# Performance work log

Measured on AMD Instinct MI355X. Metric: run time of the kernel, lower is better.

Reference implementation:

```python
import jax, jax.numpy as jnp
import numpy as np

COMMITMENT_COST = 0.25
NUM_EMBEDDINGS = 512
EMBEDDING_DIM = 64


def setup_inputs() -> dict:
    key = jax.random.key(0)
    k1, k2 = jax.random.split(key)
    B, T = 64, 1024
    inputs = jax.random.normal(k1, (B, T, EMBEDDING_DIM), dtype=jnp.float32)
    # matches nn.Embedding init uniform_(-1/K, 1/K)
    embedding = jax.random.uniform(
        k2, (NUM_EMBEDDINGS, EMBEDDING_DIM), dtype=jnp.float32,
        minval=-1.0 / NUM_EMBEDDINGS, maxval=1.0 / NUM_EMBEDDINGS)
    return {"inputs": inputs, "embedding": embedding}


def reference(inputs, embedding):
    B = inputs.shape[0]
    K, D = embedding.shape
    flat = inputs.reshape(-1, D)  # [N, D]
    # squared-euclidean distances [N, K] (same expansion as torch source)
    distances = (
        jnp.sum(flat * flat, axis=1, keepdims=True)
        + jnp.sum(embedding * embedding, axis=1)
        - 2.0 * flat @ embedding.T
    )
    idx = jnp.argmin(distances, axis=1)  # [N]
    # one-hot @ embedding  ==  gather
    quantized = embedding[idx].reshape(inputs.shape)

    e_latent_loss = jnp.mean((jax.lax.stop_gradient(quantized) - inputs) ** 2)
    q_latent_loss = jnp.mean((quantized - jax.lax.stop_gradient(inputs)) ** 2)
    loss = q_latent_loss + COMMITMENT_COST * e_latent_loss

    # straight-through estimator
    quantized_st = inputs + jax.lax.stop_gradient(quantized - inputs)

    # avg_probs = mean of one-hot encodings == histogram of indices / N
    counts = jax.ops.segment_sum(
        jnp.ones(flat.shape[0], dtype=jnp.float32), idx, num_segments=K)
    avg_probs = counts / flat.shape[0]
    perplexity = jnp.exp(-jnp.sum(avg_probs * jnp.log(avg_probs + 1e-10)))

    indices_for_transformer = idx.reshape(B, -1)
    return loss, quantized_st, perplexity, indices_for_transformer
```

## Files before the change

kernel.cpp:

```cpp
#include <hip/hip_runtime.h>
#include <math.h>

#define D 64
#define K 512
#define BLOCK 256
#define ROWS 128
#define KT 128
#define NKT (K / KT)
#define NPART 32


__device__ __forceinline__ float np_sumsq64(const float* v) {
#pragma clang fp contract(off)
    float r[8];
#pragma unroll
    for (int m = 0; m < 8; ++m) r[m] = v[m] * v[m];
#pragma unroll
    for (int i = 8; i < 64; i += 8) {
#pragma unroll
        for (int m = 0; m < 8; ++m) r[m] = r[m] + v[i + m] * v[i + m];
    }
    return ((r[0] + r[1]) + (r[2] + r[3])) + ((r[4] + r[5]) + (r[6] + r[7]));
}

__global__ __launch_bounds__(BLOCK, 2) void vq_fused(
    const float* __restrict__ x, const float* __restrict__ emb,
    float* __restrict__ q_out, float* __restrict__ idx_out,
    float* __restrict__ block_sums, int* __restrict__ part_hist, int N)
{
    __shared__ float4 xs4[ROWS * 16];
    __shared__ float4 es4[KT * 16];
    __shared__ float sx_s[ROWS];
    __shared__ float se_s[KT];
    __shared__ int hist[K];
    __shared__ float red[BLOCK / 64];

    const int tid = threadIdx.x;
    const int rg = tid & 15;
    const int cg = tid >> 4;
    const int rowbase = blockIdx.x * ROWS;

    for (int k2 = tid; k2 < K; k2 += BLOCK) hist[k2] = 0;

    const float4* xsrc = (const float4*)(x + (size_t)rowbase * D);
#pragma unroll
    for (int i = 0; i < (ROWS * 16) / BLOCK; ++i) {
        int f = tid + i * BLOCK;
        int row = f >> 4, jc = f & 15;
        xs4[row * 16 + (jc ^ ((row >> 3) & 7))] = xsrc[f];
    }
    __syncthreads();

    if (tid < ROWS) {
        float xr[D];
        const int sw = (tid >> 3) & 7;
#pragma unroll
        for (int jc = 0; jc < 16; ++jc) {
            float4 v = xs4[tid * 16 + (jc ^ sw)];
            xr[4 * jc + 0] = v.x; xr[4 * jc + 1] = v.y;
            xr[4 * jc + 2] = v.z; xr[4 * jc + 3] = v.w;
        }
        sx_s[tid] = np_sumsq64(xr);
    }

    float bd[8], bkf[8];
#pragma unroll
    for (int r = 0; r < 8; ++r) { bd[r] = INFINITY; bkf[r] = 0.f; }

    const int xbase = rg * 8, ebase = cg * 8;
    const int swx0 = rg & 7, swe0 = cg & 7;

    for (int kt = 0; kt < NKT; ++kt) {
        const float4* esrc = (const float4*)(emb + (size_t)kt * KT * D);
#pragma unroll
        for (int i = 0; i < (KT * 16) / BLOCK; ++i) {
            int f = tid + i * BLOCK;
            int row = f >> 4, jc = f & 15;
            es4[row * 16 + (jc ^ ((row >> 3) & 7))] = esrc[f];
        }
        __syncthreads();

        if (tid < KT) {
            float er[D];
            const int sw = (tid >> 3) & 7;
#pragma unroll
            for (int jc = 0; jc < 16; ++jc) {
                float4 v = es4[tid * 16 + (jc ^ sw)];
                er[4 * jc + 0] = v.x; er[4 * jc + 1] = v.y;
                er[4 * jc + 2] = v.z; er[4 * jc + 3] = v.w;
            }
            se_s[tid] = np_sumsq64(er);
        }

        float acc[8][8];
#pragma unroll
        for (int r = 0; r < 8; ++r)
#pragma unroll
            for (int c = 0; c < 8; ++c) acc[r][c] = 0.f;

#pragma unroll 2
        for (int jc = 0; jc < 16; ++jc) {
            float4 xa[8], eb[8];
#pragma unroll
            for (int r = 0; r < 8; ++r)
                xa[r] = xs4[(xbase + r) * 16 + (jc ^ swx0)];
#pragma unroll
            for (int c = 0; c < 8; ++c)
                eb[c] = es4[(ebase + c) * 16 + (jc ^ swe0)];
#pragma unroll
            for (int r = 0; r < 8; ++r)
#pragma unroll
                for (int c = 0; c < 8; ++c) {
                    acc[r][c] = fmaf(xa[r].x, eb[c].x, acc[r][c]);
                    acc[r][c] = fmaf(xa[r].y, eb[c].y, acc[r][c]);
                    acc[r][c] = fmaf(xa[r].z, eb[c].z, acc[r][c]);
                    acc[r][c] = fmaf(xa[r].w, eb[c].w, acc[r][c]);
                }
        }
        __syncthreads();

        const int kglob = kt * KT + ebase;
        float sev[8];
#pragma unroll
        for (int c = 0; c < 8; ++c) sev[c] = se_s[ebase + c];
#pragma unroll
        for (int r = 0; r < 8; ++r) {
            float sxv = sx_s[xbase + r];
#pragma unroll
            for (int c = 0; c < 8; ++c) {
                float dcur = (sxv + sev[c]) - 2.0f * acc[r][c];
                if (dcur < bd[r]) { bd[r] = dcur; bkf[r] = (float)(kglob + c); }
            }
        }
    }

    __syncthreads();
    float2* bests = (float2*)es4;
#pragma unroll
    for (int r = 0; r < 8; ++r)
        bests[(xbase + r) * 16 + cg] = make_float2(bd[r], bkf[r]);
    __syncthreads();

    float s = 0.f;
    if (tid < ROWS) {
        float bdd = INFINITY, bjf = 1e30f;
#pragma unroll
        for (int g = 0; g < 16; ++g) {
            float2 p = bests[tid * 16 + g];
            if (p.x < bdd || (p.x == bdd && p.y < bjf)) { bdd = p.x; bjf = p.y; }
        }
        const int bi = (int)bjf;
        atomicAdd(&hist[bi], 1);

        const int rowg = rowbase + tid;
        const float4* ep = (const float4*)(emb + (size_t)bi * D);
        float4* qp = (float4*)(q_out + (size_t)rowg * D);
        const int sw = (tid >> 3) & 7;
#pragma unroll
        for (int jc = 0; jc < 16; ++jc) {
            float4 xv = xs4[tid * 16 + (jc ^ sw)];
            float4 e  = ep[jc];
            float dx0 = e.x - xv.x, dx1 = e.y - xv.y;
            float dx2 = e.z - xv.z, dx3 = e.w - xv.w;
            s = fmaf(dx0, dx0, s);
            s = fmaf(dx1, dx1, s);
            s = fmaf(dx2, dx2, s);
            s = fmaf(dx3, dx3, s);
            float4 qs;
            qs.x = xv.x + dx0; qs.y = xv.y + dx1;
            qs.z = xv.z + dx2; qs.w = xv.w + dx3;
            qp[jc] = qs;
        }
        idx_out[rowg] = (float)bi;
    }

    for (int off = 32; off; off >>= 1) s += __shfl_down(s, off, 64);
    if ((tid & 63) == 0) red[tid >> 6] = s;
    __syncthreads();
    if (tid == 0) {
        float t = 0.f;
#pragma unroll
        for (int w = 0; w < BLOCK / 64; ++w) t += red[w];
        block_sums[blockIdx.x] = t;
    }
    const int part = (int)(blockIdx.x & (NPART - 1));
    for (int k2 = tid; k2 < K; k2 += BLOCK) {
        int h = hist[k2];
        if (h) atomicAdd(&part_hist[part * K + k2], h);
    }
}

__global__ __launch_bounds__(512) void vq_finalize(
    const float* __restrict__ block_sums, int nblocks,
    const int* __restrict__ part_hist, float* __restrict__ out_loss,
    float* __restrict__ out_perp, float inv_nelem, float inv_rows)
{
    const int tid = threadIdx.x;
    double ls = 0.0;
    for (int i = tid; i < nblocks; i += 512) ls += (double)block_sums[i];
    int c = 0;
#pragma unroll
    for (int pp = 0; pp < NPART; ++pp) c += part_hist[pp * K + tid];
    double ps = 0.0;
    {
        float p = (float)c * inv_rows;
        ps = (double)(p * logf(p + 1e-10f));
    }
    for (int off = 32; off; off >>= 1) {
        ls += __shfl_down(ls, off, 64);
        ps += __shfl_down(ps, off, 64);
    }
    __shared__ double l8[8], p8[8];
    if ((tid & 63) == 0) { l8[tid >> 6] = ls; p8[tid >> 6] = ps; }
    __syncthreads();
    if (tid == 0) {
        double L = 0.0, P = 0.0;
#pragma unroll
        for (int w = 0; w < 8; ++w) { L += l8[w]; P += p8[w]; }
        *out_loss = 1.25f * (float)(L * (double)inv_nelem);
        *out_perp = expf((float)(-P));
    }
}

extern "C" void kernel_launch(void* const* d_in, const int* in_sizes, int n_in,
                              void* d_out, int out_size, void* d_ws, size_t ws_size,
                              hipStream_t stream) {
    const float* x   = (const float*)d_in[0];
    const float* emb = (const float*)d_in[1];
    const int N = in_sizes[0] / D;
    const int nblocks = N / ROWS;

    float* out      = (float*)d_out;
    float* loss_out = out;
    float* q_out    = out + 1;
    float* perp_out = out + 1 + (size_t)N * D;
    float* idx_out  = perp_out + 1;

    float* block_sums = (float*)d_ws;
    int*   part_hist  = (int*)((char*)d_ws + (((size_t)nblocks * 4 + 255) & ~(size_t)255));

    hipMemsetAsync(part_hist, 0, NPART * K * sizeof(int), stream);
    vq_fused<<<nblocks, BLOCK, 0, stream>>>(x, emb, q_out, idx_out,
                                            block_sums, part_hist, N);
    vq_finalize<<<1, 512, 0, stream>>>(block_sums, nblocks, part_hist,
                                       loss_out, perp_out,
                                       1.0f / (float)((size_t)N * D),
                                       1.0f / (float)N);
}
```

Baseline: 139.8 us.

## Fuse finalize into main kernel, stream codebook from global, shuffle-reduce argmin

Removes the shared-memory codebook tile staging and per-tile barriers. Each thread now reads its 8 codebook rows straight from global/L2 and precomputes all codebook norms up front. The per-row argmin is reduced across column groups with wave shuffles instead of a 16-way shared-memory scan. The separate finalize kernel is folded into the main kernel through a last-block-done atomic counter, which saves one launch. The cost is that direct global loads of the codebook may have higher latency than LDS reads, and each block redundantly computes all 512 codebook norms.

Result: slower. 204.9 us (+46.6%).

```diff
diff --git a/kernel.cpp b/kernel.cpp
--- a/kernel.cpp
+++ b/kernel.cpp
@@ -5,8 +5,7 @@
 #define K 512
 #define BLOCK 256
 #define ROWS 128
-#define KT 128
-#define NKT (K / KT)
+#define NTILE 4
 #define NPART 32
 
 
@@ -26,16 +25,23 @@
 __global__ __launch_bounds__(BLOCK, 2) void vq_fused(
     const float* __restrict__ x, const float* __restrict__ emb,
     float* __restrict__ q_out, float* __restrict__ idx_out,
-    float* __restrict__ block_sums, int* __restrict__ part_hist, int N)
+    float* __restrict__ block_sums, int* __restrict__ part_hist,
+    int* __restrict__ done_ctr,
+    float* __restrict__ out_loss, float* __restrict__ out_perp,
+    float inv_nelem, float inv_rows)
 {
     __shared__ float4 xs4[ROWS * 16];
-    __shared__ float4 es4[KT * 16];
     __shared__ float sx_s[ROWS];
-    __shared__ float se_s[KT];
+    __shared__ float se_s[K];
+    __shared__ float2 bests[4 * ROWS];
     __shared__ int hist[K];
-    __shared__ float red[BLOCK / 64];
+    __shared__ float redf[BLOCK / 64];
+    __shared__ double l8[BLOCK / 64], p8[BLOCK / 64];
+    __shared__ int flag_s;
 
     const int tid = threadIdx.x;
+    const int lane = tid & 63;
+    const int wv = tid >> 6;
     const int rg = tid & 15;
     const int cg = tid >> 4;
     const int rowbase = blockIdx.x * ROWS;
@@ -49,104 +55,134 @@
         int row = f >> 4, jc = f & 15;
         xs4[row * 16 + (jc ^ ((row >> 3) & 7))] = xsrc[f];
     }
-    __syncthreads();
+
+#pragma unroll
+    for (int t = 0; t < K / BLOCK; ++t) {
+        const int k0 = tid + t * BLOCK;
+        float er[D];
+        const float4* e4 = (const float4*)(emb + (size_t)k0 * D);
+#pragma unroll
+        for (int j = 0; j < 16; ++j) {
+            float4 v = e4[j];
+            er[4 * j + 0] = v.x; er[4 * j + 1] = v.y;
+            er[4 * j + 2] = v.z; er[4 * j + 3] = v.w;
+        }
+        se_s[k0] = np_sumsq64(er);
+    }
 
     if (tid < ROWS) {
         float xr[D];
-        const int sw = (tid >> 3) & 7;
-#pragma unroll
+        const float4* xp = (const float4*)(x + (size_t)(rowbase + tid) * D);
+#pragma unroll
+        for (int j = 0; j < 16; ++j) {
+            float4 v = xp[j];
+            xr[4 * j + 0] = v.x; xr[4 * j + 1] = v.y;
+            xr[4 * j + 2] = v.z; xr[4 * j + 3] = v.w;
+        }
+        sx_s[tid] = np_sumsq64(xr);
+    }
+    __syncthreads();
+
+    float bd[8], bkf[8];
+#pragma unroll
+    for (int r = 0; r < 8; ++r) { bd[r] = INFINITY; bkf[r] = 0.f; }
+
+    const int xbase = rg * 8;
+    const int sw = rg & 7;
+
+#pragma unroll 1
+    for (int t = 0; t < NTILE; ++t) {
+        const int kb = t * 128 + cg * 8;
+        const float4* ebase = (const float4*)(emb + (size_t)kb * D);
+
+        float acc[8][8];
+#pragma unroll
+        for (int r = 0; r < 8; ++r)
+#pragma unroll
+            for (int c = 0; c < 8; ++c) acc[r][c] = 0.f;
+
+#pragma unroll 4
         for (int jc = 0; jc < 16; ++jc) {
-            float4 v = xs4[tid * 16 + (jc ^ sw)];
-            xr[4 * jc + 0] = v.x; xr[4 * jc + 1] = v.y;
-            xr[4 * jc + 2] = v.z; xr[4 * jc + 3] = v.w;
-        }
-        sx_s[tid] = np_sumsq64(xr);
-    }
-
-    float bd[8], bkf[8];
-#pragma unroll
-    for (int r = 0; r < 8; ++r) { bd[r] = INFINITY; bkf[r] = 0.f; }
-
-    const int xbase = rg * 8, ebase = cg * 8;
-    const int swx0 = rg & 7, swe0 = cg & 7;
-
-    for (int kt = 0; kt < NKT; ++kt) {
-        const float4* esrc = (const float4*)(emb + (size_t)kt * KT * D);
-#pragma unroll
-        for (int i = 0; i < (KT * 16) / BLOCK; ++i) {
-            int f = tid + i * BLOCK;
-            int row = f >> 4, jc = f & 15;
-            es4[row * 16 + (jc ^ ((row >> 3) & 7))] = esrc[f];
-        }
-        __syncthreads();
-
-        if (tid < KT) {
-            float er[D];
-            const int sw = (tid >> 3) & 7;
-#pragma unroll
-            for (int jc = 0; jc < 16; ++jc) {
-                float4 v = es4[tid * 16 + (jc ^ sw)];
-                er[4 * jc + 0] = v.x; er[4 * jc + 1] = v.y;
-                er[4 * jc + 2] = v.z; er[4 * jc + 3] = v.w;
+            float4 xa[8];
+#pragma unroll
+            for (int r = 0; r < 8; ++r)
+                xa[r] = xs4[(xbase + r) * 16 + (jc ^ sw)];
+#pragma unroll
+            for (int c = 0; c < 8; ++c) {
+                const float4 ev = ebase[c * 16 + jc];
+                acc[0][c] = fmaf(xa[0].x, ev.x, acc[0][c]);
+                acc[1][c] = fmaf(xa[1].x, ev.x, acc[1][c]);
+                acc[2][c] = fmaf(xa[2].x, ev.x, acc[2][c]);
+                acc[3][c] = fmaf(xa[3].x, ev.x, acc[3][c]);
+                acc[4][c] = fmaf(xa[4].x, ev.x, acc[4][c]);
+                acc[5][c] = fmaf(xa[5].x, ev.x, acc[5][c]);
+                acc[6][c] = fmaf(xa[6].x, ev.x, acc[6][c]);
+                acc[7][c] = fmaf(xa[7].x, ev.x, acc[7][c]);
+                acc[0][c] = fmaf(xa[0].y, ev.y, acc[0][c]);
+                acc[1][c] = fmaf(xa[1].y, ev.y, acc[1][c]);
+                acc[2][c] = fmaf(xa[2].y, ev.y, acc[2][c]);
+                acc[3][c] = fmaf(xa[3].y, ev.y, acc[3][c]);
+                acc[4][c] = fmaf(xa[4].y, ev.y, acc[4][c]);
+                acc[5][c] = fmaf(xa[5].y, ev.y, acc[5][c]);
+                acc[6][c] = fmaf(xa[6].y, ev.y, acc[6][c]);
+                acc[7][c] = fmaf(xa[7].y, ev.y, acc[7][c]);
+                acc[0][c] = fmaf(xa[0].z, ev.z, acc[0][c]);
+                acc[1][c] = fmaf(xa[1].z, ev.z, acc[1][c]);
+                acc[2][c] = fmaf(xa[2].z, ev.z, acc[2][c]);
+                acc[3][c] = fmaf(xa[3].z, ev.z, acc[3][c]);
+                acc[4][c] = fmaf(xa[4].z, ev.z, acc[4][c]);
+                acc[5][c] = fmaf(xa[5].z, ev.z, acc[5][c]);
+                acc[6][c] = fmaf(xa[6].z, ev.z, acc[6][c]);
+                acc[7][c] = fmaf(xa[7].z, ev.z, acc[7][c]);
+                acc[0][c] = fmaf(xa[0].w, ev.w, acc[0][c]);
+                acc[1][c] = fmaf(xa[1].w, ev.w, acc[1][c]);
+                acc[2][c] = fmaf(xa[2].w, ev.w, acc[2][c]);
+                acc[3][c] = fmaf(xa[3].w, ev.w, acc[3][c]);
+                acc[4][c] = fmaf(xa[4].w, ev.w, acc[4][c]);
+                acc[5][c] = fmaf(xa[5].w, ev.w, acc[5][c]);
+                acc[6][c] = fmaf(xa[6].w, ev.w, acc[6][c]);
+                acc[7][c] = fmaf(xa[7].w, ev.w, acc[7][c]);
             }
-            se_s[tid] = np_sumsq64(er);
-        }
-
-        float acc[8][8];
-#pragma unroll
-        for (int r = 0; r < 8; ++r)
-#pragma unroll
-            for (int c = 0; c < 8; ++c) acc[r][c] = 0.f;
-
-#pragma unroll 2
-        for (int jc = 0; jc < 16; ++jc) {
-            float4 xa[8], eb[8];
-#pragma unroll
-            for (int r = 0; r < 8; ++r)
-                xa[r] = xs4[(xbase + r) * 16 + (jc ^ swx0)];
-#pragma unroll
-            for (int c = 0; c < 8; ++c)
-                eb[c] = es4[(ebase + c) * 16 + (jc ^ swe0)];
-#pragma unroll
-            for (int r = 0; r < 8; ++r)
-#pragma unroll
-                for (int c = 0; c < 8; ++c) {
-                    acc[r][c] = fmaf(xa[r].x, eb[c].x, acc[r][c]);
-                    acc[r][c] = fmaf(xa[r].y, eb[c].y, acc[r][c]);
-                    acc[r][c] = fmaf(xa[r].z, eb[c].z, acc[r][c]);
-                    acc[r][c] = fmaf(xa[r].w, eb[c].w, acc[r][c]);
-                }
-        }
-        __syncthreads();
-
-        const int kglob = kt * KT + ebase;
+        }
+
         float sev[8];
 #pragma unroll
-        for (int c = 0; c < 8; ++c) sev[c] = se_s[ebase + c];
+        for (int c = 0; c < 8; ++c) sev[c] = se_s[kb + c];
 #pragma unroll
         for (int r = 0; r < 8; ++r) {
-            float sxv = sx_s[xbase + r];
+            const float sxv = sx_s[xbase + r];
 #pragma unroll
             for (int c = 0; c < 8; ++c) {
                 float dcur = (sxv + sev[c]) - 2.0f * acc[r][c];
-                if (dcur < bd[r]) { bd[r] = dcur; bkf[r] = (float)(kglob + c); }
+                if (dcur < bd[r]) { bd[r] = dcur; bkf[r] = (float)(kb + c); }
             }
         }
     }
 
-    __syncthreads();
-    float2* bests = (float2*)es4;
-#pragma unroll
-    for (int r = 0; r < 8; ++r)
-        bests[(xbase + r) * 16 + cg] = make_float2(bd[r], bkf[r]);
+#pragma unroll
+    for (int off = 16; off <= 32; off <<= 1) {
+#pragma unroll
+        for (int r = 0; r < 8; ++r) {
+            float od = __shfl_xor(bd[r], off, 64);
+            float ok = __shfl_xor(bkf[r], off, 64);
+            if (od < bd[r] || (od == bd[r] && ok < bkf[r])) {
+                bd[r] = od; bkf[r] = ok;
+            }
+        }
+    }
+    if (lane < 16) {
+#pragma unroll
+        for (int r = 0; r < 8; ++r)
+            bests[wv * ROWS + lane * 8 + r] = make_float2(bd[r], bkf[r]);
+    }
     __syncthreads();
 
     float s = 0.f;
     if (tid < ROWS) {
         float bdd = INFINITY, bjf = 1e30f;
 #pragma unroll
-        for (int g = 0; g < 16; ++g) {
-            float2 p = bests[tid * 16 + g];
+        for (int w = 0; w < 4; ++w) {
+            float2 p = bests[w * ROWS + tid];
             if (p.x < bdd || (p.x == bdd && p.y < bjf)) { bdd = p.x; bjf = p.y; }
         }
         const int bi = (int)bjf;
@@ -155,10 +191,10 @@
         const int rowg = rowbase + tid;
         const float4* ep = (const float4*)(emb + (size_t)bi * D);
         float4* qp = (float4*)(q_out + (size_t)rowg * D);
-        const int sw = (tid >> 3) & 7;
+        const int esw = (tid >> 3) & 7;
 #pragma unroll
         for (int jc = 0; jc < 16; ++jc) {
-            float4 xv = xs4[tid * 16 + (jc ^ sw)];
+            float4 xv = xs4[tid * 16 + (jc ^ esw)];
             float4 e  = ep[jc];
             float dx0 = e.x - xv.x, dx1 = e.y - xv.y;
             float dx2 = e.z - xv.z, dx3 = e.w - xv.w;
@@ -175,48 +211,53 @@
     }
 
     for (int off = 32; off; off >>= 1) s += __shfl_down(s, off, 64);
-    if ((tid & 63) == 0) red[tid >> 6] = s;
+    if (lane == 0) redf[wv] = s;
     __syncthreads();
     if (tid == 0) {
-        float t = 0.f;
-#pragma unroll
-        for (int w = 0; w < BLOCK / 64; ++w) t += red[w];
-        block_sums[blockIdx.x] = t;
-    }
+        float tsum = 0.f;
+#pragma unroll
+        for (int w = 0; w < BLOCK / 64; ++w) tsum += redf[w];
+        block_sums[blockIdx.x] = tsum;
+    }
+
     const int part = (int)(blockIdx.x & (NPART - 1));
     for (int k2 = tid; k2 < K; k2 += BLOCK) {
         int h = hist[k2];
         if (h) atomicAdd(&part_hist[part * K + k2], h);
     }
-}
-
-__global__ __launch_bounds__(512) void vq_finalize(
-    const float* __restrict__ block_sums, int nblocks,
-    const int* __restrict__ part_hist, float* __restrict__ out_loss,
-    float* __restrict__ out_perp, float inv_nelem, float inv_rows)
-{
-    const int tid = threadIdx.x;
+
+    __threadfence();
+    __syncthreads();
+    if (tid == 0) flag_s = atomicAdd(done_ctr, 1);
+    __syncthreads();
+    if (flag_s != (int)gridDim.x - 1) return;
+
+    __threadfence();
+    const int nblocks = (int)gridDim.x;
     double ls = 0.0;
-    for (int i = tid; i < nblocks; i += 512) ls += (double)block_sums[i];
-    int c = 0;
-#pragma unroll
-    for (int pp = 0; pp < NPART; ++pp) c += part_hist[pp * K + tid];
+    for (int i = tid; i < nblocks; i += BLOCK)
+        ls += (double)__hip_atomic_load(&block_sums[i], __ATOMIC_RELAXED,
+                                        __HIP_MEMORY_SCOPE_AGENT);
     double ps = 0.0;
-    {
-        float p = (float)c * inv_rows;
-        ps = (double)(p * logf(p + 1e-10f));
+    for (int k2 = tid; k2 < K; k2 += BLOCK) {
+        int c = 0;
+#pragma unroll
+        for (int p = 0; p < NPART; ++p)
+            c += __hip_atomic_load(&part_hist[p * K + k2], __ATOMIC_RELAXED,
+                                   __HIP_MEMORY_SCOPE_AGENT);
+        float pv = (float)c * inv_rows;
+        ps += (double)(pv * logf(pv + 1e-10f));
     }
     for (int off = 32; off; off >>= 1) {
         ls += __shfl_down(ls, off, 64);
         ps += __shfl_down(ps, off, 64);
     }
-    __shared__ double l8[8], p8[8];
-    if ((tid & 63) == 0) { l8[tid >> 6] = ls; p8[tid >> 6] = ps; }
+    if (lane == 0) { l8[wv] = ls; p8[wv] = ps; }
     __syncthreads();
     if (tid == 0) {
         double L = 0.0, P = 0.0;
 #pragma unroll
-        for (int w = 0; w < 8; ++w) { L += l8[w]; P += p8[w]; }
+        for (int w = 0; w < BLOCK / 64; ++w) { L += l8[w]; P += p8[w]; }
         *out_loss = 1.25f * (float)(L * (double)inv_nelem);
         *out_perp = expf((float)(-P));
     }
@@ -237,13 +278,15 @@
     float* idx_out  = perp_out + 1;
 
     float* block_sums = (float*)d_ws;
-    int*   part_hist  = (int*)((char*)d_ws + (((size_t)nblocks * 4 + 255) & ~(size_t)255));
-
-    hipMemsetAsync(part_hist, 0, NPART * K * sizeof(int), stream);
+    int*   part_hist  = (int*)((char*)d_ws +
+                               (((size_t)nblocks * 4 + 255) & ~(size_t)255));
+    int*   done_ctr   = part_hist + (size_t)NPART * K;
+
+    hipMemsetAsync(part_hist, 0, (size_t)NPART * K * sizeof(int) + sizeof(int),
+                   stream);
     vq_fused<<<nblocks, BLOCK, 0, stream>>>(x, emb, q_out, idx_out,
-                                            block_sums, part_hist, N);
-    vq_finalize<<<1, 512, 0, stream>>>(block_sums, nblocks, part_hist,
-                                       loss_out, perp_out,
-                                       1.0f / (float)((size_t)N * D),
-                                       1.0f / (float)N);
+                                            block_sums, part_hist, done_ctr,
+                                            loss_out, perp_out,
+                                            1.0f / (float)((size_t)N * D),
+                                            1.0f / (float)N);
 }
```
